# Kernel tuning notes

Hardware: AMD Instinct MI355X
Metric: run time of the kernel (lower is better)

The kernel has to match this reference:

```python
import jax, jax.numpy as jnp
import numpy as np

N_CHANNELS = 32
DIM_CAPSULE = 16


def setup_inputs() -> dict:
    key = jax.random.key(0)
    k1, k2, k3 = jax.random.split(key, 3)
    B, H, W, Cin = 32, 56, 56, 256
    d, n = DIM_CAPSULE, N_CHANNELS
    inputs = jax.random.normal(k1, (B, H, W, Cin), dtype=jnp.float32)
    # glorot-ish scale for the 3x3 conv kernel
    convW_1 = jax.random.normal(k2, (3, 3, Cin, d * n), dtype=jnp.float32) * 0.02
    bias_1 = jnp.zeros((d * n,), dtype=jnp.float32)
    CapsAct_W = jax.random.normal(k3, (1, 1, d, d * n), dtype=jnp.float32) * 0.1
    CapsAct_B = jnp.zeros((d * n,), dtype=jnp.float32)
    return {"inputs": inputs, "convW_1": convW_1, "bias_1": bias_1,
            "CapsAct_W": CapsAct_W, "CapsAct_B": CapsAct_B}


def reference(inputs, convW_1, bias_1, CapsAct_W, CapsAct_B):
    d, n = DIM_CAPSULE, N_CHANNELS
    # 3x3 stride-2 SAME conv (NHWC / HWIO), bias, relu
    y = jax.lax.conv_general_dilated(
        inputs, convW_1, window_strides=(2, 2), padding="SAME",
        dimension_numbers=("NHWC", "HWIO", "NHWC"))
    y = jax.nn.relu(y + bias_1)                      # [B, Ho, Wo, d*n]
    B, Ho, Wo, _ = y.shape
    # Per-channel 1x1 convs == grouped matmul over capsule channels.
    yg = y.reshape(B, Ho, Wo, n, d)                  # group channels: [B,Ho,Wo,n,d_in]
    Wg = CapsAct_W.reshape(d, n, d)                  # [d_in, n, d_out]
    bg = CapsAct_B.reshape(n, d)                     # [n, d_out]
    # output layout matches tf: [B, Ho, Wo, dim_capsule, n_channels]
    out = jnp.einsum("bhwnd,dne->bhwen", yg, Wg) + bg.T[None, None, None]
    return out
```

## Files before the change

kernel.cpp:

```cpp
#include <hip/hip_runtime.h>
#include <hip/hip_bf16.h>

typedef __attribute__((ext_vector_type(4))) float f32x4;
typedef __attribute__((ext_vector_type(8))) short s16x8;
typedef __attribute__((ext_vector_type(8))) unsigned short u16x8;
typedef __attribute__((ext_vector_type(4))) unsigned short u16x4;

__device__ __forceinline__ unsigned short bfbits(float f) {
  unsigned int u = __builtin_bit_cast(unsigned int, f);
  return (unsigned short)((u + 0x8000u) >> 16);
}

__device__ __forceinline__ void gll16(void* lds, const void* g) {
  __builtin_amdgcn_global_load_lds(
      (const __attribute__((address_space(1))) unsigned int*)g,
      (__attribute__((address_space(3))) unsigned int*)lds, 16, 0, 0);
}

__global__ void prep_weights(const float* __restrict__ w,
                             __hip_bfloat16* __restrict__ wt) {
  int u = blockIdx.x * 256 + threadIdx.x;
  int n = u & 511;
  int c8 = (u >> 9) & 31;
  int kpos = u >> 14;
  int t = kpos * 8 + (c8 >> 2);
  int cq = c8 & 3;
  const float* src = w + ((kpos * 256 + c8 * 8) * 512) + n;
  u16x8 d;
#pragma unroll
  for (int j = 0; j < 8; ++j) d[j] = bfbits(src[j * 512]);
  int nb = n >> 7, nl = n & 127;
  *reinterpret_cast<u16x8*>(wt + ((t * 4 + nb) * 4096 + cq * 1024 + nl * 8)) = d;
}

__global__ __launch_bounds__(256)
void prep_input_t(const float* __restrict__ in, __hip_bfloat16* __restrict__ dst) {
  __shared__ __align__(16) unsigned short row[14848];
  int bh = blockIdx.x;
  int h = bh % 57, b = bh / 57;
  int t = threadIdx.x;
  __hip_bfloat16* d = (__hip_bfloat16*)dst + (long)bh * 14848;
  if (h < 56) {
    if (t < 64) {
      int par = t >> 5, cq = t & 31;
      u16x4 z = {0, 0, 0, 0};
      *(u16x4*)(row + (par * 32 + cq) * 232 + 224) = z;
      *(u16x4*)(row + (par * 32 + cq) * 232 + 228) = z;
    }
    const float* src = in + (long)(b * 56 + h) * 56 * 256;
#pragma unroll
    for (int j = 0; j < 14; ++j) {
      int idx = j * 256 + t;
      f32x4 v = *(const f32x4*)(src + idx * 4);
      int e0 = idx * 4;
      int w = e0 >> 8, c = e0 & 255;
      int off = ((w & 1) * 32 + (c >> 3)) * 232 + (w >> 1) * 8 + (c & 7);
      u16x4 q = {bfbits(v[0]), bfbits(v[1]), bfbits(v[2]), bfbits(v[3])};
      *(u16x4*)(row + off) = q;
    }
    __syncthreads();
    for (int i = t; i < 1856; i += 256)
      *(u16x8*)(d + i * 8) = *(const u16x8*)(row + i * 8);
  } else {
    u16x8 z = {0, 0, 0, 0, 0, 0, 0, 0};
    for (int i = t; i < 1856; i += 256) *(u16x8*)(d + i * 8) = z;
  }
}

__global__ __launch_bounds__(512, 4)
void caps_main_fast(const __hip_bfloat16* __restrict__ inp,
                    const __hip_bfloat16* __restrict__ wt,
                    const float* __restrict__ bias1,
                    const float* __restrict__ capsW,
                    const float* __restrict__ capsB,
                    float* __restrict__ out) {
  __shared__ __align__(16) unsigned char smem[73728];

  int bid = (int)blockIdx.x;
  bid = (bid & 7) * 49 + (bid >> 3);
  int mblk = bid >> 2;
  int nb = bid & 3;
  int p0 = mblk * 256;

  int tid = threadIdx.x;
  int lane = tid & 63;
  int wv = tid >> 6;
  int wm = (wv >> 1) * 64;
  int wn = (wv & 1) * 64;
  int col = lane & 15;
  int lq = lane >> 4;

  int mq = wv >> 1;
  int cqa = (wv & 1) * 2;
  int bcq = wv >> 1;
  int bnh = wv & 1;

  int p = p0 + mq * 64 + lane;
  int b = p / 784;
  int rr = p - b * 784;
  int ho = rr / 28;
  int wo = rr - ho * 28;
  int base0 = b * 846336 + 2 * ho * 14848 + wo * 8;

  const __hip_bfloat16* wtb = wt + nb * 4096;

  f32x4 acc[4][4] = {};

  auto stage = [&](int buf, int t) {
    int kp = t >> 3, tc = t & 7;
    int kh = (kp * 11) >> 5;
    int kw = kp - kh * 3;
    __hip_bfloat16* sa = (__hip_bfloat16*)smem + buf * 12288;
    __hip_bfloat16* sb = sa + 8192;
    const __hip_bfloat16* as =
        inp + base0 + kh * 14848 + (kw & 1) * 7424 + (kw >> 1) * 8 + (tc * 4 + cqa) * 232;
    gll16(sa + cqa * 2048 + mq * 512, as);
    gll16(sa + (cqa + 1) * 2048 + mq * 512, as + 232);
    const __hip_bfloat16* bs = wtb + t * 16384 + bcq * 1024 + bnh * 512 + lane * 8;
    gll16(sb + bcq * 1024 + bnh * 512, bs);
  };

  stage(0, 0);
  stage(1, 1);
  __asm__ volatile("s_waitcnt vmcnt(3)" ::: "memory");
  __builtin_amdgcn_s_barrier();

  int rd = 0;
  for (int t = 0; t < 72; ++t) {
    const __hip_bfloat16* sa = (const __hip_bfloat16*)smem + rd * 12288;
    const __hip_bfloat16* sb = sa + 8192;
    s16x8 af[4], bfr[4];
#pragma unroll
    for (int mf = 0; mf < 4; ++mf)
      af[mf] = *(const s16x8*)(sa + lq * 2048 + (wm + 16 * mf + col) * 8);
#pragma unroll
    for (int nf = 0; nf < 4; ++nf)
      bfr[nf] = *(const s16x8*)(sb + lq * 1024 + (wn + 16 * nf + col) * 8);
    if (t + 2 < 72) {
      int st = rd + 2; if (st >= 3) st -= 3;
      stage(st, t + 2);
    }
#pragma unroll
    for (int mf = 0; mf < 4; ++mf)
#pragma unroll
      for (int nf = 0; nf < 4; ++nf)
        acc[mf][nf] = __builtin_amdgcn_mfma_f32_16x16x32_bf16(
            af[mf], bfr[nf], acc[mf][nf], 0, 0, 0);
    if (t < 70) {
      __asm__ volatile("s_waitcnt vmcnt(3)" ::: "memory");
    } else {
      __asm__ volatile("s_waitcnt vmcnt(0)" ::: "memory");
    }
    __builtin_amdgcn_s_barrier();
    rd = (rd + 1 == 3) ? 0 : rd + 1;
  }

  __hip_bfloat16* yw = (__hip_bfloat16*)smem + wv * 4096;
  int nBase = nb * 128 + wn;
#pragma unroll
  for (int nf = 0; nf < 4; ++nf) {
    float b1v = bias1[nBase + nf * 16 + col];
#pragma unroll
    for (int mf = 0; mf < 4; ++mf) {
      f32x4 a = acc[mf][nf];
#pragma unroll
      for (int r = 0; r < 4; ++r) {
        int pl = mf * 16 + lq * 4 + r;
        int nl = nf * 16 + col;
        float v = a[r] + b1v;
        v = v > 0.f ? v : 0.f;
        int off = (pl * 128 + nl * 2) ^ ((pl & 7) << 4);
        *(unsigned short*)((char*)yw + off) = bfbits(v);
      }
    }
  }

  int gb = nb * 8 + (wv & 1) * 4;
  s16x8 wf[4];
  f32x4 cinit[4];
#pragma unroll
  for (int g = 0; g < 4; ++g) {
    int gg = gb + g;
    s16x8 bw = {0, 0, 0, 0, 0, 0, 0, 0};
    if (lq < 2) {
#pragma unroll
      for (int j = 0; j < 8; ++j)
        bw[j] = (short)bfbits(capsW[(8 * lq + j) * 512 + gg * 16 + col]);
    }
    wf[g] = bw;
    float cb = capsB[gg * 16 + col];
    cinit[g] = f32x4{cb, cb, cb, cb};
  }
#pragma unroll
  for (int mf = 0; mf < 4; ++mf) {
    int prow = 16 * mf + col;
    f32x4 dd[4];
#pragma unroll
    for (int g = 0; g < 4; ++g) {
      s16x8 afv = {0, 0, 0, 0, 0, 0, 0, 0};
      if (lq < 2) {
        int off = (prow * 128 + g * 32 + lq * 16) ^ ((prow & 7) << 4);
        afv = *(const s16x8*)((char*)yw + off);
      }
      dd[g] = __builtin_amdgcn_mfma_f32_16x16x32_bf16(afv, wf[g], cinit[g], 0, 0, 0);
    }
    long pgl = (long)(p0 + wm) + 16 * mf;
#pragma unroll
    for (int r = 0; r < 4; ++r) {
      long pg = pgl + 4 * lq + r;
      f32x4 o = {dd[0][r], dd[1][r], dd[2][r], dd[3][r]};
      *(f32x4*)(out + (pg * 16 + col) * 32 + gb) = o;
    }
  }
}

__global__ __launch_bounds__(256, 3)
void caps_main_v1(const float* __restrict__ in, const __hip_bfloat16* __restrict__ wt,
                  const float* __restrict__ bias1, const float* __restrict__ capsW,
                  const float* __restrict__ capsB, float* __restrict__ out) {
  __shared__ __align__(16) unsigned char smem[32768];
  __hip_bfloat16* sA = (__hip_bfloat16*)smem;
  __hip_bfloat16* sB = (__hip_bfloat16*)(smem + 8192);

  int bid = (int)blockIdx.x;
  bid = (bid & 7) * 98 + (bid >> 3);
  int mblk = bid >> 2;
  int nb = bid & 3;
  int p0 = mblk * 128;

  int tid = threadIdx.x;
  int lane = tid & 63;
  int wv = tid >> 6;
  int wm = (wv >> 1) * 64;
  int wn = (wv & 1) * 64;
  int col = lane & 15;
  int lq = lane >> 4;

  int am = tid & 127;
  int ah = tid >> 7;
  int p = p0 + am;
  int bb = p / 784;
  int rr = p - bb * 784;
  int ho = rr / 28;
  int wo = rr - ho * 28;

  f32x4 acc[4][4] = {};
  const __hip_bfloat16* wtb = wt + nb * 4096;

  for (int kp = 0; kp < 9; ++kp) {
    int kh = kp / 3;
    int kw = kp - kh * 3;
    int h = 2 * ho + kh, ww = 2 * wo + kw;
    bool valid = (h < 56) && (ww < 56);
    const float* arow = in + (((bb * 56 + h) * 56 + ww) * 256) + ah * 16;
#pragma unroll
    for (int tc = 0; tc < 8; ++tc) {
      int t = kp * 8 + tc;
      __syncthreads();
      const __hip_bfloat16* bsrc = wtb + t * 16384 + tid * 8;
      gll16(sB + (wv * 512), bsrc);
      gll16(sB + 2048 + (wv * 512), bsrc + 2048);
      f32x4 v0, v1, v2, v3;
      if (valid) {
        const f32x4* apv = (const f32x4*)(arow + tc * 32);
        v0 = apv[0]; v1 = apv[1]; v2 = apv[2]; v3 = apv[3];
      } else {
        v0 = f32x4{0.f, 0.f, 0.f, 0.f}; v1 = v0; v2 = v0; v3 = v0;
      }
      u16x8 pk0, pk1;
#pragma unroll
      for (int j = 0; j < 4; ++j) {
        pk0[j] = bfbits(v0[j]); pk0[j + 4] = bfbits(v1[j]);
        pk1[j] = bfbits(v2[j]); pk1[j + 4] = bfbits(v3[j]);
      }
      *(u16x8*)(sA + (ah * 2) * 1024 + am * 8) = pk0;
      *(u16x8*)(sA + (ah * 2 + 1) * 1024 + am * 8) = pk1;
      __syncthreads();
      s16x8 af[4], bfr[4];
#pragma unroll
      for (int mf = 0; mf < 4; ++mf)
        af[mf] = *(const s16x8*)(sA + lq * 1024 + (wm + 16 * mf + col) * 8);
#pragma unroll
      for (int nf = 0; nf < 4; ++nf)
        bfr[nf] = *(const s16x8*)(sB + lq * 1024 + (wn + 16 * nf + col) * 8);
#pragma unroll
      for (int mf = 0; mf < 4; ++mf)
#pragma unroll
        for (int nf = 0; nf < 4; ++nf)
          acc[mf][nf] = __builtin_amdgcn_mfma_f32_16x16x32_bf16(
              af[mf], bfr[nf], acc[mf][nf], 0, 0, 0);
    }
  }

  __syncthreads();

  __hip_bfloat16* yw = (__hip_bfloat16*)smem + wv * 4096;
  int nBase = nb * 128 + wn;
#pragma unroll
  for (int nf = 0; nf < 4; ++nf) {
    float b1v = bias1[nBase + nf * 16 + col];
#pragma unroll
    for (int mf = 0; mf < 4; ++mf) {
      f32x4 a = acc[mf][nf];
#pragma unroll
      for (int r = 0; r < 4; ++r) {
        int pl = mf * 16 + lq * 4 + r;
        int nl = nf * 16 + col;
        float v = a[r] + b1v;
        v = v > 0.f ? v : 0.f;
        int off = (pl * 128 + nl * 2) ^ ((pl & 7) << 4);
        *(unsigned short*)((char*)yw + off) = bfbits(v);
      }
    }
  }

  int gb = nb * 8 + (wv & 1) * 4;
  s16x8 wf[4];
  f32x4 cinit[4];
#pragma unroll
  for (int g = 0; g < 4; ++g) {
    int gg = gb + g;
    s16x8 bw = {0, 0, 0, 0, 0, 0, 0, 0};
    if (lq < 2) {
#pragma unroll
      for (int j = 0; j < 8; ++j)
        bw[j] = (short)bfbits(capsW[(8 * lq + j) * 512 + gg * 16 + col]);
    }
    wf[g] = bw;
    float cb = capsB[gg * 16 + col];
    cinit[g] = f32x4{cb, cb, cb, cb};
  }
#pragma unroll
  for (int mf = 0; mf < 4; ++mf) {
    int prow = 16 * mf + col;
    f32x4 dd[4];
#pragma unroll
    for (int g = 0; g < 4; ++g) {
      s16x8 afv = {0, 0, 0, 0, 0, 0, 0, 0};
      if (lq < 2) {
        int off = (prow * 128 + g * 32 + lq * 16) ^ ((prow & 7) << 4);
        afv = *(const s16x8*)((char*)yw + off);
      }
      dd[g] = __builtin_amdgcn_mfma_f32_16x16x32_bf16(afv, wf[g], cinit[g], 0, 0, 0);
    }
    long pgl = (long)(p0 + wm) + 16 * mf;
#pragma unroll
    for (int r = 0; r < 4; ++r) {
      long pg = pgl + 4 * lq + r;
      f32x4 o = {dd[0][r], dd[1][r], dd[2][r], dd[3][r]};
      *(f32x4*)(out + (pg * 16 + col) * 32 + gb) = o;
    }
  }
}

extern "C" void kernel_launch(void* const* d_in, const int* in_sizes, int n_in,
                              void* d_out, int out_size, void* d_ws, size_t ws_size,
                              hipStream_t stream) {
  const float* inputs = (const float*)d_in[0];
  const float* convW  = (const float*)d_in[1];
  const float* bias1  = (const float*)d_in[2];
  const float* capsW  = (const float*)d_in[3];
  const float* capsB  = (const float*)d_in[4];
  float* out = (float*)d_out;

  __hip_bfloat16* wt = (__hip_bfloat16*)d_ws;
  const size_t IN_OFF = 2621440;
  const size_t NEED = IN_OFF + (size_t)27082752 * 2;

  prep_weights<<<576, 256, 0, stream>>>(convW, wt);
  if (ws_size >= NEED) {
    __hip_bfloat16* inp = (__hip_bfloat16*)((char*)d_ws + IN_OFF);
    prep_input_t<<<1824, 256, 0, stream>>>(inputs, inp);
    caps_main_fast<<<392, 512, 0, stream>>>(inp, wt, bias1, capsW, capsB, out);
  } else {
    caps_main_v1<<<784, 256, 0, stream>>>(inputs, wt, bias1, capsW, capsB, out);
  }
}
```

Measured before the change: 109.7 us.

## Halve GEMM block tile and deepen LDS pipeline with register double-buffering

Shrinks the main conv-GEMM kernel from 512-thread blocks with a 256-row tile to 256-thread blocks with a 128-row tile, doubling the grid. It moves from a 3-stage to a 4-stage LDS ring and double-buffers the A/B fragments in registers, so LDS reads for the next step are issued before the current MFMAs. It also raises wave priority around the MFMA burst. The aim is better latency hiding and load balance across CUs, at the cost of more global/LDS traffic per output from the smaller tile and higher register pressure.

```diff
diff --git a/kernel.cpp b/kernel.cpp
--- a/kernel.cpp
+++ b/kernel.cpp
@@ -67,20 +67,20 @@
   }
 }
 
-__global__ __launch_bounds__(512, 4)
+__global__ __launch_bounds__(256, 2)
 void caps_main_fast(const __hip_bfloat16* __restrict__ inp,
                     const __hip_bfloat16* __restrict__ wt,
                     const float* __restrict__ bias1,
                     const float* __restrict__ capsW,
                     const float* __restrict__ capsB,
                     float* __restrict__ out) {
-  __shared__ __align__(16) unsigned char smem[73728];
+  __shared__ __align__(16) unsigned char smem[65536];
 
   int bid = (int)blockIdx.x;
-  bid = (bid & 7) * 49 + (bid >> 3);
+  bid = (bid & 7) * 98 + (bid >> 3);
   int mblk = bid >> 2;
   int nb = bid & 3;
-  int p0 = mblk * 256;
+  int p0 = mblk * 128;
 
   int tid = threadIdx.x;
   int lane = tid & 63;
@@ -90,17 +90,14 @@
   int col = lane & 15;
   int lq = lane >> 4;
 
-  int mq = wv >> 1;
-  int cqa = (wv & 1) * 2;
-  int bcq = wv >> 1;
-  int bnh = wv & 1;
-
-  int p = p0 + mq * 64 + lane;
-  int b = p / 784;
-  int rr = p - b * 784;
-  int ho = rr / 28;
-  int wo = rr - ho * 28;
-  int base0 = b * 846336 + 2 * ho * 14848 + wo * 8;
+  int pA0 = p0 + lane;
+  int pA1 = p0 + 64 + lane;
+  int b0 = pA0 / 784, r0 = pA0 - b0 * 784;
+  int h0 = r0 / 28, w0 = r0 - h0 * 28;
+  int baseA0 = b0 * 846336 + 2 * h0 * 14848 + w0 * 8;
+  int b1 = pA1 / 784, r1 = pA1 - b1 * 784;
+  int h1 = r1 / 28, w1 = r1 - h1 * 28;
+  int baseA1 = b1 * 846336 + 2 * h1 * 14848 + w1 * 8;
 
   const __hip_bfloat16* wtb = wt + nb * 4096;
 
@@ -110,49 +107,67 @@
     int kp = t >> 3, tc = t & 7;
     int kh = (kp * 11) >> 5;
     int kw = kp - kh * 3;
-    __hip_bfloat16* sa = (__hip_bfloat16*)smem + buf * 12288;
-    __hip_bfloat16* sb = sa + 8192;
-    const __hip_bfloat16* as =
-        inp + base0 + kh * 14848 + (kw & 1) * 7424 + (kw >> 1) * 8 + (tc * 4 + cqa) * 232;
-    gll16(sa + cqa * 2048 + mq * 512, as);
-    gll16(sa + (cqa + 1) * 2048 + mq * 512, as + 232);
-    const __hip_bfloat16* bs = wtb + t * 16384 + bcq * 1024 + bnh * 512 + lane * 8;
-    gll16(sb + bcq * 1024 + bnh * 512, bs);
+    int koff = kh * 14848 + (kw & 1) * 7424 + (kw >> 1) * 8 + (tc * 4 + wv) * 232;
+    __hip_bfloat16* sa = (__hip_bfloat16*)(smem + buf * 16384) + wv * 1024;
+    gll16(sa, inp + baseA0 + koff);
+    gll16(sa + 512, inp + baseA1 + koff);
+    __hip_bfloat16* sb = (__hip_bfloat16*)(smem + buf * 16384) + 4096 + wv * 1024;
+    const __hip_bfloat16* bs = wtb + t * 16384 + wv * 1024 + lane * 8;
+    gll16(sb, bs);
+    gll16(sb + 512, bs + 512);
   };
+
+  auto rdfrag = [&](int buf, s16x8 (&a)[4], s16x8 (&bf)[4]) {
+    const __hip_bfloat16* sa = (const __hip_bfloat16*)(smem + buf * 16384);
+    const __hip_bfloat16* sb = sa + 4096;
+#pragma unroll
+    for (int mf = 0; mf < 4; ++mf)
+      a[mf] = *(const s16x8*)(sa + lq * 1024 + (wm + 16 * mf + col) * 8);
+#pragma unroll
+    for (int nf = 0; nf < 4; ++nf)
+      bf[nf] = *(const s16x8*)(sb + lq * 1024 + (wn + 16 * nf + col) * 8);
+  };
+
+  s16x8 a0[4], bq0[4], a1[4], bq1[4];
 
   stage(0, 0);
   stage(1, 1);
-  __asm__ volatile("s_waitcnt vmcnt(3)" ::: "memory");
+  stage(2, 2);
+  __asm__ volatile("s_waitcnt vmcnt(4)" ::: "memory");
   __builtin_amdgcn_s_barrier();
-
-  int rd = 0;
-  for (int t = 0; t < 72; ++t) {
-    const __hip_bfloat16* sa = (const __hip_bfloat16*)smem + rd * 12288;
-    const __hip_bfloat16* sb = sa + 8192;
-    s16x8 af[4], bfr[4];
-#pragma unroll
-    for (int mf = 0; mf < 4; ++mf)
-      af[mf] = *(const s16x8*)(sa + lq * 2048 + (wm + 16 * mf + col) * 8);
-#pragma unroll
-    for (int nf = 0; nf < 4; ++nf)
-      bfr[nf] = *(const s16x8*)(sb + lq * 1024 + (wn + 16 * nf + col) * 8);
-    if (t + 2 < 72) {
-      int st = rd + 2; if (st >= 3) st -= 3;
-      stage(st, t + 2);
-    }
+  __asm__ volatile("" ::: "memory");
+  rdfrag(0, a0, bq0);
+
+  auto halfstep = [&](int t, s16x8 (&ac)[4], s16x8 (&bc)[4],
+                      s16x8 (&an)[4], s16x8 (&bn)[4]) {
+    if (t + 3 < 72) stage((t + 3) & 3, t + 3);
+    if (t + 1 < 72) {
+      rdfrag((t + 1) & 3, an, bn);
+      __asm__ volatile("s_waitcnt lgkmcnt(8)" ::: "memory");
+    } else {
+      __asm__ volatile("s_waitcnt lgkmcnt(0)" ::: "memory");
+    }
+    __builtin_amdgcn_sched_barrier(0);
+    __builtin_amdgcn_s_setprio(1);
 #pragma unroll
     for (int mf = 0; mf < 4; ++mf)
 #pragma unroll
       for (int nf = 0; nf < 4; ++nf)
         acc[mf][nf] = __builtin_amdgcn_mfma_f32_16x16x32_bf16(
-            af[mf], bfr[nf], acc[mf][nf], 0, 0, 0);
-    if (t < 70) {
-      __asm__ volatile("s_waitcnt vmcnt(3)" ::: "memory");
+            ac[mf], bc[nf], acc[mf][nf], 0, 0, 0);
+    __builtin_amdgcn_s_setprio(0);
+    if (t < 69) {
+      __asm__ volatile("s_waitcnt vmcnt(4)" ::: "memory");
     } else {
       __asm__ volatile("s_waitcnt vmcnt(0)" ::: "memory");
     }
     __builtin_amdgcn_s_barrier();
-    rd = (rd + 1 == 3) ? 0 : rd + 1;
+    __asm__ volatile("" ::: "memory");
+  };
+
+  for (int t = 0; t < 72; t += 2) {
+    halfstep(t, a0, bq0, a1, bq1);
+    halfstep(t + 1, a1, bq1, a0, bq0);
   }
 
   __hip_bfloat16* yw = (__hip_bfloat16*)smem + wv * 4096;
@@ -371,7 +386,7 @@
   if (ws_size >= NEED) {
     __hip_bfloat16* inp = (__hip_bfloat16*)((char*)d_ws + IN_OFF);
     prep_input_t<<<1824, 256, 0, stream>>>(inputs, inp);
-    caps_main_fast<<<392, 512, 0, stream>>>(inp, wt, bias1, capsW, capsB, out);
+    caps_main_fast<<<784, 256, 0, stream>>>(inp, wt, bias1, capsW, capsB, out);
   } else {
     caps_main_v1<<<784, 256, 0, stream>>>(inputs, wt, bias1, capsW, capsB, out);
   }
```

Result: slower. 119.5 us (+8.9%).

## Halve main GEMM block tile to 128x128 with 256 threads and 784 blocks

Applied to the files above, without the earlier changes.

Shrinks each workgroup of the fused conv+capsule kernel from 8 waves over a 256-pixel tile to 4 waves over a 128-pixel tile. The grid doubles to 784 blocks and LDS per block drops to 48KB, so more blocks fit per CU and the 256 CUs get better wave balance than with 392 blocks. Staging is rewritten so each wave loads two A rows and two B chunks, with the wait counts adjusted to match. The epilogue gains an extra barrier before reusing the staging LDS, and the bias loads are hoisted. In exchange, each B tile is reused across fewer pixels, so there are more global weight reads per FLOP.

```diff
diff --git a/kernel.cpp b/kernel.cpp
--- a/kernel.cpp
+++ b/kernel.cpp
@@ -67,20 +67,20 @@
   }
 }
 
-__global__ __launch_bounds__(512, 4)
+__global__ __launch_bounds__(256, 3)
 void caps_main_fast(const __hip_bfloat16* __restrict__ inp,
                     const __hip_bfloat16* __restrict__ wt,
                     const float* __restrict__ bias1,
                     const float* __restrict__ capsW,
                     const float* __restrict__ capsB,
                     float* __restrict__ out) {
-  __shared__ __align__(16) unsigned char smem[73728];
+  __shared__ __align__(16) unsigned char smem[49152];
 
   int bid = (int)blockIdx.x;
-  bid = (bid & 7) * 49 + (bid >> 3);
+  bid = (bid & 7) * 98 + (bid >> 3);
   int mblk = bid >> 2;
   int nb = bid & 3;
-  int p0 = mblk * 256;
+  int p0 = mblk * 128;
 
   int tid = threadIdx.x;
   int lane = tid & 63;
@@ -90,17 +90,14 @@
   int col = lane & 15;
   int lq = lane >> 4;
 
-  int mq = wv >> 1;
-  int cqa = (wv & 1) * 2;
-  int bcq = wv >> 1;
-  int bnh = wv & 1;
-
-  int p = p0 + mq * 64 + lane;
-  int b = p / 784;
-  int rr = p - b * 784;
-  int ho = rr / 28;
-  int wo = rr - ho * 28;
-  int base0 = b * 846336 + 2 * ho * 14848 + wo * 8;
+  int px0 = p0 + lane;
+  int px1 = p0 + 64 + lane;
+  int b0 = px0 / 784, r0 = px0 - b0 * 784;
+  int h0 = r0 / 28, w0 = r0 - h0 * 28;
+  int baseA0 = b0 * 846336 + 2 * h0 * 14848 + w0 * 8;
+  int b1 = px1 / 784, r1 = px1 - b1 * 784;
+  int h1 = r1 / 28, w1 = r1 - h1 * 28;
+  int baseA1 = b1 * 846336 + 2 * h1 * 14848 + w1 * 8;
 
   const __hip_bfloat16* wtb = wt + nb * 4096;
 
@@ -110,29 +107,30 @@
     int kp = t >> 3, tc = t & 7;
     int kh = (kp * 11) >> 5;
     int kw = kp - kh * 3;
-    __hip_bfloat16* sa = (__hip_bfloat16*)smem + buf * 12288;
-    __hip_bfloat16* sb = sa + 8192;
-    const __hip_bfloat16* as =
-        inp + base0 + kh * 14848 + (kw & 1) * 7424 + (kw >> 1) * 8 + (tc * 4 + cqa) * 232;
-    gll16(sa + cqa * 2048 + mq * 512, as);
-    gll16(sa + (cqa + 1) * 2048 + mq * 512, as + 232);
-    const __hip_bfloat16* bs = wtb + t * 16384 + bcq * 1024 + bnh * 512 + lane * 8;
-    gll16(sb + bcq * 1024 + bnh * 512, bs);
+    int koff = kh * 14848 + (kw & 1) * 7424 + (kw >> 1) * 8 + (tc * 4 + wv) * 232;
+    __hip_bfloat16* sa = (__hip_bfloat16*)(smem + buf * 16384);
+    gll16(sa + wv * 1024, inp + baseA0 + koff);
+    gll16(sa + wv * 1024 + 512, inp + baseA1 + koff);
+    __hip_bfloat16* sb = sa + 4096;
+    const __hip_bfloat16* bs = wtb + t * 16384 + wv * 1024 + lane * 8;
+    gll16(sb + wv * 1024, bs);
+    gll16(sb + wv * 1024 + 512, bs + 512);
   };
 
   stage(0, 0);
   stage(1, 1);
-  __asm__ volatile("s_waitcnt vmcnt(3)" ::: "memory");
+  __asm__ volatile("s_waitcnt vmcnt(4)" ::: "memory");
   __builtin_amdgcn_s_barrier();
+  __asm__ volatile("" ::: "memory");
 
   int rd = 0;
   for (int t = 0; t < 72; ++t) {
-    const __hip_bfloat16* sa = (const __hip_bfloat16*)smem + rd * 12288;
-    const __hip_bfloat16* sb = sa + 8192;
+    const __hip_bfloat16* sa = (const __hip_bfloat16*)(smem + rd * 16384);
+    const __hip_bfloat16* sb = sa + 4096;
     s16x8 af[4], bfr[4];
 #pragma unroll
     for (int mf = 0; mf < 4; ++mf)
-      af[mf] = *(const s16x8*)(sa + lq * 2048 + (wm + 16 * mf + col) * 8);
+      af[mf] = *(const s16x8*)(sa + lq * 1024 + (wm + 16 * mf + col) * 8);
 #pragma unroll
     for (int nf = 0; nf < 4; ++nf)
       bfr[nf] = *(const s16x8*)(sb + lq * 1024 + (wn + 16 * nf + col) * 8);
@@ -147,32 +145,13 @@
         acc[mf][nf] = __builtin_amdgcn_mfma_f32_16x16x32_bf16(
             af[mf], bfr[nf], acc[mf][nf], 0, 0, 0);
     if (t < 70) {
-      __asm__ volatile("s_waitcnt vmcnt(3)" ::: "memory");
-    } else {
+      __asm__ volatile("s_waitcnt vmcnt(4)" ::: "memory");
+    } else if (t == 70) {
       __asm__ volatile("s_waitcnt vmcnt(0)" ::: "memory");
     }
     __builtin_amdgcn_s_barrier();
+    __asm__ volatile("" ::: "memory");
     rd = (rd + 1 == 3) ? 0 : rd + 1;
-  }
-
-  __hip_bfloat16* yw = (__hip_bfloat16*)smem + wv * 4096;
-  int nBase = nb * 128 + wn;
-#pragma unroll
-  for (int nf = 0; nf < 4; ++nf) {
-    float b1v = bias1[nBase + nf * 16 + col];
-#pragma unroll
-    for (int mf = 0; mf < 4; ++mf) {
-      f32x4 a = acc[mf][nf];
-#pragma unroll
-      for (int r = 0; r < 4; ++r) {
-        int pl = mf * 16 + lq * 4 + r;
-        int nl = nf * 16 + col;
-        float v = a[r] + b1v;
-        v = v > 0.f ? v : 0.f;
-        int off = (pl * 128 + nl * 2) ^ ((pl & 7) << 4);
-        *(unsigned short*)((char*)yw + off) = bfbits(v);
-      }
-    }
   }
 
   int gb = nb * 8 + (wv & 1) * 4;
@@ -191,6 +170,34 @@
     float cb = capsB[gg * 16 + col];
     cinit[g] = f32x4{cb, cb, cb, cb};
   }
+  float b1v[4];
+  int nBase = nb * 128 + wn;
+#pragma unroll
+  for (int nf = 0; nf < 4; ++nf) b1v[nf] = bias1[nBase + nf * 16 + col];
+
+  __asm__ volatile("s_waitcnt vmcnt(0) lgkmcnt(0)" ::: "memory");
+  __builtin_amdgcn_s_barrier();
+  __asm__ volatile("" ::: "memory");
+
+  __hip_bfloat16* yw = (__hip_bfloat16*)smem + wv * 4096;
+#pragma unroll
+  for (int nf = 0; nf < 4; ++nf) {
+#pragma unroll
+    for (int mf = 0; mf < 4; ++mf) {
+      f32x4 a = acc[mf][nf];
+#pragma unroll
+      for (int r = 0; r < 4; ++r) {
+        int pl = mf * 16 + lq * 4 + r;
+        int nl = nf * 16 + col;
+        float v = a[r] + b1v[nf];
+        v = v > 0.f ? v : 0.f;
+        int off = (pl * 128 + nl * 2) ^ ((pl & 7) << 4);
+        *(unsigned short*)((char*)yw + off) = bfbits(v);
+      }
+    }
+  }
+  __asm__ volatile("s_waitcnt lgkmcnt(0)" ::: "memory");
+
 #pragma unroll
   for (int mf = 0; mf < 4; ++mf) {
     int prow = 16 * mf + col;
@@ -371,7 +378,7 @@
   if (ws_size >= NEED) {
     __hip_bfloat16* inp = (__hip_bfloat16*)((char*)d_ws + IN_OFF);
     prep_input_t<<<1824, 256, 0, stream>>>(inputs, inp);
-    caps_main_fast<<<392, 512, 0, stream>>>(inp, wt, bias1, capsW, capsB, out);
+    caps_main_fast<<<784, 256, 0, stream>>>(inp, wt, bias1, capsW, capsB, out);
   } else {
     caps_main_v1<<<784, 256, 0, stream>>>(inputs, wt, bias1, capsW, capsB, out);
   }
```

After: 122.2 us. +11.4%, slower.

## Fuse prep kernels and interleave LDS fragment loads with MFMA issue

Applied to the files above, without the earlier changes.

The weight and input bf16 conversion kernels are merged into one launch, so one launch and its inter-kernel gap go away. In the main GEMM loop, fragment reads are split: the first two A fragments and all B fragments are read before the async stage, and the last two A fragments after it. Scheduling barriers, partial lgkmcnt waits and s_setprio around the MFMA groups let the first eight MFMAs start while the later LDS reads are still in flight. The fallback path now runs the combined prep kernel and writes the full converted input to the start of the workspace. That overlaps the weight buffer and likely overflows a small workspace, so the fallback is risky.

```diff
diff --git a/kernel.cpp b/kernel.cpp
--- a/kernel.cpp
+++ b/kernel.cpp
@@ -17,53 +17,53 @@
       (__attribute__((address_space(3))) unsigned int*)lds, 16, 0, 0);
 }
 
-__global__ void prep_weights(const float* __restrict__ w,
-                             __hip_bfloat16* __restrict__ wt) {
-  int u = blockIdx.x * 256 + threadIdx.x;
-  int n = u & 511;
-  int c8 = (u >> 9) & 31;
-  int kpos = u >> 14;
-  int t = kpos * 8 + (c8 >> 2);
-  int cq = c8 & 3;
-  const float* src = w + ((kpos * 256 + c8 * 8) * 512) + n;
-  u16x8 d;
-#pragma unroll
-  for (int j = 0; j < 8; ++j) d[j] = bfbits(src[j * 512]);
-  int nb = n >> 7, nl = n & 127;
-  *reinterpret_cast<u16x8*>(wt + ((t * 4 + nb) * 4096 + cq * 1024 + nl * 8)) = d;
-}
-
 __global__ __launch_bounds__(256)
-void prep_input_t(const float* __restrict__ in, __hip_bfloat16* __restrict__ dst) {
-  __shared__ __align__(16) unsigned short row[14848];
-  int bh = blockIdx.x;
-  int h = bh % 57, b = bh / 57;
+void prep_all(const float* __restrict__ in, __hip_bfloat16* __restrict__ dst,
+              const float* __restrict__ w, __hip_bfloat16* __restrict__ wt) {
   int t = threadIdx.x;
-  __hip_bfloat16* d = (__hip_bfloat16*)dst + (long)bh * 14848;
-  if (h < 56) {
-    if (t < 64) {
-      int par = t >> 5, cq = t & 31;
-      u16x4 z = {0, 0, 0, 0};
-      *(u16x4*)(row + (par * 32 + cq) * 232 + 224) = z;
-      *(u16x4*)(row + (par * 32 + cq) * 232 + 228) = z;
-    }
-    const float* src = in + (long)(b * 56 + h) * 56 * 256;
-#pragma unroll
-    for (int j = 0; j < 14; ++j) {
-      int idx = j * 256 + t;
-      f32x4 v = *(const f32x4*)(src + idx * 4);
-      int e0 = idx * 4;
-      int w = e0 >> 8, c = e0 & 255;
-      int off = ((w & 1) * 32 + (c >> 3)) * 232 + (w >> 1) * 8 + (c & 7);
-      u16x4 q = {bfbits(v[0]), bfbits(v[1]), bfbits(v[2]), bfbits(v[3])};
-      *(u16x4*)(row + off) = q;
-    }
-    __syncthreads();
-    for (int i = t; i < 1856; i += 256)
-      *(u16x8*)(d + i * 8) = *(const u16x8*)(row + i * 8);
+  if (blockIdx.x < 1824) {
+    __shared__ __align__(16) unsigned short row[14848];
+    int bh = blockIdx.x;
+    int h = bh % 57, b = bh / 57;
+    __hip_bfloat16* d = (__hip_bfloat16*)dst + (long)bh * 14848;
+    if (h < 56) {
+      if (t < 64) {
+        int par = t >> 5, cq = t & 31;
+        u16x4 z = {0, 0, 0, 0};
+        *(u16x4*)(row + (par * 32 + cq) * 232 + 224) = z;
+        *(u16x4*)(row + (par * 32 + cq) * 232 + 228) = z;
+      }
+      const float* src = in + (long)(b * 56 + h) * 56 * 256;
+#pragma unroll
+      for (int j = 0; j < 14; ++j) {
+        int idx = j * 256 + t;
+        f32x4 v = *(const f32x4*)(src + idx * 4);
+        int e0 = idx * 4;
+        int ww = e0 >> 8, c = e0 & 255;
+        int off = ((ww & 1) * 32 + (c >> 3)) * 232 + (ww >> 1) * 8 + (c & 7);
+        u16x4 q = {bfbits(v[0]), bfbits(v[1]), bfbits(v[2]), bfbits(v[3])};
+        *(u16x4*)(row + off) = q;
+      }
+      __syncthreads();
+      for (int i = t; i < 1856; i += 256)
+        *(u16x8*)(d + i * 8) = *(const u16x8*)(row + i * 8);
+    } else {
+      u16x8 z = {0, 0, 0, 0, 0, 0, 0, 0};
+      for (int i = t; i < 1856; i += 256) *(u16x8*)(d + i * 8) = z;
+    }
   } else {
-    u16x8 z = {0, 0, 0, 0, 0, 0, 0, 0};
-    for (int i = t; i < 1856; i += 256) *(u16x8*)(d + i * 8) = z;
+    int u = (blockIdx.x - 1824) * 256 + t;
+    int n = u & 511;
+    int c8 = (u >> 9) & 31;
+    int kpos = u >> 14;
+    int tt = kpos * 8 + (c8 >> 2);
+    int cq = c8 & 3;
+    const float* src = w + ((kpos * 256 + c8 * 8) * 512) + n;
+    u16x8 d;
+#pragma unroll
+    for (int j = 0; j < 8; ++j) d[j] = bfbits(src[j * 512]);
+    int nb = n >> 7, nl = n & 127;
+    *reinterpret_cast<u16x8*>(wt + ((tt * 4 + nb) * 4096 + cq * 1024 + nl * 8)) = d;
   }
 }
 
@@ -75,6 +75,7 @@
                     const float* __restrict__ capsB,
                     float* __restrict__ out) {
   __shared__ __align__(16) unsigned char smem[73728];
+  __hip_bfloat16* smem_e = (__hip_bfloat16*)smem;
 
   int bid = (int)blockIdx.x;
   bid = (bid & 7) * 49 + (bid >> 3);
@@ -110,7 +111,7 @@
     int kp = t >> 3, tc = t & 7;
     int kh = (kp * 11) >> 5;
     int kw = kp - kh * 3;
-    __hip_bfloat16* sa = (__hip_bfloat16*)smem + buf * 12288;
+    __hip_bfloat16* sa = smem_e + buf * 12288;
     __hip_bfloat16* sb = sa + 8192;
     const __hip_bfloat16* as =
         inp + base0 + kh * 14848 + (kw & 1) * 7424 + (kw >> 1) * 8 + (tc * 4 + cqa) * 232;
@@ -124,38 +125,61 @@
   stage(1, 1);
   __asm__ volatile("s_waitcnt vmcnt(3)" ::: "memory");
   __builtin_amdgcn_s_barrier();
+  __asm__ volatile("" ::: "memory");
 
   int rd = 0;
   for (int t = 0; t < 72; ++t) {
-    const __hip_bfloat16* sa = (const __hip_bfloat16*)smem + rd * 12288;
+    const __hip_bfloat16* sa = smem_e + rd * 12288;
     const __hip_bfloat16* sb = sa + 8192;
-    s16x8 af[4], bfr[4];
-#pragma unroll
-    for (int mf = 0; mf < 4; ++mf)
-      af[mf] = *(const s16x8*)(sa + lq * 2048 + (wm + 16 * mf + col) * 8);
-#pragma unroll
-    for (int nf = 0; nf < 4; ++nf)
-      bfr[nf] = *(const s16x8*)(sb + lq * 1024 + (wn + 16 * nf + col) * 8);
+    s16x8 af0 = *(const s16x8*)(sa + lq * 2048 + (wm + 0 + col) * 8);
+    s16x8 af1 = *(const s16x8*)(sa + lq * 2048 + (wm + 16 + col) * 8);
+    s16x8 b0 = *(const s16x8*)(sb + lq * 1024 + (wn + 0 + col) * 8);
+    s16x8 b1 = *(const s16x8*)(sb + lq * 1024 + (wn + 16 + col) * 8);
+    s16x8 b2 = *(const s16x8*)(sb + lq * 1024 + (wn + 32 + col) * 8);
+    s16x8 b3 = *(const s16x8*)(sb + lq * 1024 + (wn + 48 + col) * 8);
+    __builtin_amdgcn_sched_barrier(0);
     if (t + 2 < 72) {
       int st = rd + 2; if (st >= 3) st -= 3;
       stage(st, t + 2);
     }
-#pragma unroll
-    for (int mf = 0; mf < 4; ++mf)
-#pragma unroll
-      for (int nf = 0; nf < 4; ++nf)
-        acc[mf][nf] = __builtin_amdgcn_mfma_f32_16x16x32_bf16(
-            af[mf], bfr[nf], acc[mf][nf], 0, 0, 0);
+    s16x8 af2 = *(const s16x8*)(sa + lq * 2048 + (wm + 32 + col) * 8);
+    s16x8 af3 = *(const s16x8*)(sa + lq * 2048 + (wm + 48 + col) * 8);
+    __builtin_amdgcn_sched_barrier(0);
+    __asm__ volatile("s_waitcnt lgkmcnt(2)" ::: "memory");
+    __builtin_amdgcn_sched_barrier(0);
+    __builtin_amdgcn_s_setprio(1);
+    acc[0][0] = __builtin_amdgcn_mfma_f32_16x16x32_bf16(af0, b0, acc[0][0], 0, 0, 0);
+    acc[0][1] = __builtin_amdgcn_mfma_f32_16x16x32_bf16(af0, b1, acc[0][1], 0, 0, 0);
+    acc[0][2] = __builtin_amdgcn_mfma_f32_16x16x32_bf16(af0, b2, acc[0][2], 0, 0, 0);
+    acc[0][3] = __builtin_amdgcn_mfma_f32_16x16x32_bf16(af0, b3, acc[0][3], 0, 0, 0);
+    acc[1][0] = __builtin_amdgcn_mfma_f32_16x16x32_bf16(af1, b0, acc[1][0], 0, 0, 0);
+    acc[1][1] = __builtin_amdgcn_mfma_f32_16x16x32_bf16(af1, b1, acc[1][1], 0, 0, 0);
+    acc[1][2] = __builtin_amdgcn_mfma_f32_16x16x32_bf16(af1, b2, acc[1][2], 0, 0, 0);
+    acc[1][3] = __builtin_amdgcn_mfma_f32_16x16x32_bf16(af1, b3, acc[1][3], 0, 0, 0);
+    __builtin_amdgcn_s_setprio(0);
+    __asm__ volatile("s_waitcnt lgkmcnt(0)" ::: "memory");
+    __builtin_amdgcn_sched_barrier(0);
+    __builtin_amdgcn_s_setprio(1);
+    acc[2][0] = __builtin_amdgcn_mfma_f32_16x16x32_bf16(af2, b0, acc[2][0], 0, 0, 0);
+    acc[2][1] = __builtin_amdgcn_mfma_f32_16x16x32_bf16(af2, b1, acc[2][1], 0, 0, 0);
+    acc[2][2] = __builtin_amdgcn_mfma_f32_16x16x32_bf16(af2, b2, acc[2][2], 0, 0, 0);
+    acc[2][3] = __builtin_amdgcn_mfma_f32_16x16x32_bf16(af2, b3, acc[2][3], 0, 0, 0);
+    acc[3][0] = __builtin_amdgcn_mfma_f32_16x16x32_bf16(af3, b0, acc[3][0], 0, 0, 0);
+    acc[3][1] = __builtin_amdgcn_mfma_f32_16x16x32_bf16(af3, b1, acc[3][1], 0, 0, 0);
+    acc[3][2] = __builtin_amdgcn_mfma_f32_16x16x32_bf16(af3, b2, acc[3][2], 0, 0, 0);
+    acc[3][3] = __builtin_amdgcn_mfma_f32_16x16x32_bf16(af3, b3, acc[3][3], 0, 0, 0);
+    __builtin_amdgcn_s_setprio(0);
     if (t < 70) {
       __asm__ volatile("s_waitcnt vmcnt(3)" ::: "memory");
-    } else {
+    } else if (t == 70) {
       __asm__ volatile("s_waitcnt vmcnt(0)" ::: "memory");
     }
     __builtin_amdgcn_s_barrier();
+    __asm__ volatile("" ::: "memory");
     rd = (rd + 1 == 3) ? 0 : rd + 1;
   }
 
-  __hip_bfloat16* yw = (__hip_bfloat16*)smem + wv * 4096;
+  __hip_bfloat16* yw = smem_e + wv * 4096;
   int nBase = nb * 128 + wn;
 #pragma unroll
   for (int nf = 0; nf < 4; ++nf) {
@@ -367,12 +391,12 @@
   const size_t IN_OFF = 2621440;
   const size_t NEED = IN_OFF + (size_t)27082752 * 2;
 
-  prep_weights<<<576, 256, 0, stream>>>(convW, wt);
   if (ws_size >= NEED) {
     __hip_bfloat16* inp = (__hip_bfloat16*)((char*)d_ws + IN_OFF);
-    prep_input_t<<<1824, 256, 0, stream>>>(inputs, inp);
+    prep_all<<<2400, 256, 0, stream>>>(inputs, inp, convW, wt);
     caps_main_fast<<<392, 512, 0, stream>>>(inp, wt, bias1, capsW, capsB, out);
   } else {
+    prep_all<<<2400, 256, 0, stream>>>(inputs, (__hip_bfloat16*)d_ws, convW, wt);
     caps_main_v1<<<784, 256, 0, stream>>>(inputs, wt, bias1, capsW, capsB, out);
   }
 }
```

Result: faster. 103.9 us (-5.3%).
